# Kernel tuning notes

Hardware: AMD Instinct MI355X
Metric: run time of the kernel (lower is better)

Reference implementation:

```python
import jax, jax.numpy as jnp
import numpy as np

BN_EPS = 1e-5
L2_EPS = 1e-12


def _gconv(x, adj, W, b):
    # x: [B, N, F_in], adj: [N, N] (densified sparse), W: [F_in, F_out]
    y = jnp.einsum('rc,bcf->brf', adj, x)          # sparse aggregation (spmm)
    y = jnp.einsum('brf,fo->bro', y, W) + b        # dense transform + bias
    n = jnp.sqrt(jnp.sum(y * y, axis=2, keepdims=True))
    return y / jnp.maximum(n, L2_EPS)              # F.normalize(p=2, dim=2)


def _bn3(x):
    # BatchNorm1d over channel dim=1 (roinum), batch stats, affine = identity
    m = jnp.mean(x, axis=(0, 2), keepdims=True)
    v = jnp.var(x, axis=(0, 2), keepdims=True)
    return (x - m) / jnp.sqrt(v + BN_EPS)


def _bn2(x):
    m = jnp.mean(x, axis=0, keepdims=True)
    v = jnp.var(x, axis=0, keepdims=True)
    return (x - m) / jnp.sqrt(v + BN_EPS)


def setup_inputs() -> dict:
    key = jax.random.key(0)
    ks = jax.random.split(key, 20)
    B, N, F_in, H, E, L = 256, 400, 400, 64, 64, 2
    NNZ = 16000
    pred_in = H * 2 + E  # hidden*(num_layers-1) + embedding = 192
    nhid = H

    def xavier(k, fi, fo):
        s = np.sqrt(6.0 / (fi + fo))
        return jax.random.uniform(k, (fi, fo), jnp.float32, -s, s)

    return {
        'x': jax.random.normal(ks[0], (B, N, F_in), jnp.float32),
        'adj_rows': jax.random.randint(ks[1], (NNZ,), 0, N, jnp.int32),
        'adj_cols': jax.random.randint(ks[2], (NNZ,), 0, N, jnp.int32),
        'adj_vals': jax.random.uniform(ks[3], (NNZ,), jnp.float32),
        'W1': xavier(ks[4], F_in, H), 'b1': jnp.zeros((H,), jnp.float32),
        'W2': xavier(ks[5], H, H),    'b2': jnp.zeros((H,), jnp.float32),
        'W3': xavier(ks[6], H, E),    'b3': jnp.zeros((E,), jnp.float32),
        'fc1_W': xavier(ks[7], pred_in, nhid), 'fc1_b': jnp.zeros((nhid,), jnp.float32),
        'fc2_W': xavier(ks[8], nhid, nhid),    'fc2_b': jnp.zeros((nhid,), jnp.float32),
        'fc3_W': xavier(ks[9], nhid, L),       'fc3_b': jnp.zeros((L,), jnp.float32),
    }


def reference(x, adj_rows, adj_cols, adj_vals,
              W1, b1, W2, b2, W3, b3,
              fc1_W, fc1_b, fc2_W, fc2_b, fc3_W, fc3_b):
    N = x.shape[1]
    adj = jnp.zeros((N, N), x.dtype).at[adj_rows, adj_cols].add(adj_vals)

    x1 = _bn3(jax.nn.relu(_gconv(x, adj, W1, b1)))
    out1 = jnp.max(x1, axis=1)                     # [B, H]
    x2 = _bn3(jax.nn.relu(_gconv(x1, adj, W2, b2)))
    out2 = jnp.max(x2, axis=1)                     # [B, H]
    x3 = _gconv(x2, adj, W3, b3)                   # [B, N, E]
    out3 = jnp.max(x3, axis=1)                     # [B, E]

    h = jnp.concatenate([out1, out2, out3], axis=1)  # [B, 2H+E]
    h = _bn2(jax.nn.relu(h @ fc1_W + fc1_b))
    h = _bn2(jax.nn.relu(h @ fc2_W + fc2_b))
    ypred = h @ fc3_W + fc3_b
    return ypred, x3
```

## Files before the change

### kernel.cpp

```cpp
#include <hip/hip_runtime.h>
#include <hip/hip_bf16.h>
#include <math.h>

#define Bb   256
#define Nn   400
#define FIN  400
#define Hh   64
#define NNZ  16000
#define Mrows (Bb*Nn)
#define KP   416
#define UTP  416
#define BH_COUNT 16384.0f

typedef unsigned int  u32x2 __attribute__((ext_vector_type(2)));
typedef unsigned int  u32x4 __attribute__((ext_vector_type(4)));
typedef __bf16        bf16x8 __attribute__((ext_vector_type(8)));
typedef float         f32x4 __attribute__((ext_vector_type(4)));

__device__ __forceinline__ unsigned int f2bf(float x) {
    unsigned int u = __builtin_bit_cast(unsigned int, x);
    return (u + 0x7FFFu + ((u >> 16) & 1u)) >> 16;
}
__device__ __forceinline__ float bf2f(unsigned int h) {
    unsigned int u = h << 16;
    return __builtin_bit_cast(float, u);
}

__global__ void initk(float* __restrict__ Adf, float* __restrict__ stats,
                      unsigned short* __restrict__ Ut) {
    int t = blockIdx.x * blockDim.x + threadIdx.x;
    if (t < Nn * KP) Adf[t] = 0.f;
    if (t < 1600) stats[t] = 0.f;
    if (t < Bb * Hh * 16) {
        int bh = t >> 4, k = Nn + (t & 15);
        Ut[(size_t)bh * UTP + k] = 0;
    }
}

__global__ void scatAk(const int* __restrict__ rows, const int* __restrict__ cols,
                       const float* __restrict__ vals, float* __restrict__ Adf) {
    int i = blockIdx.x * blockDim.x + threadIdx.x;
    if (i < NNZ) atomicAdd(&Adf[rows[i] * KP + cols[i]], vals[i]);
}

__global__ void cvtAk(const float* __restrict__ Adf, unsigned short* __restrict__ Adbf) {
    int i = blockIdx.x * blockDim.x + threadIdx.x;
    if (i < Nn * KP) Adbf[i] = (unsigned short)f2bf(Adf[i]);
}

__global__ __launch_bounds__(256) void wprep(
        const float* __restrict__ W1, const float* __restrict__ W2,
        const float* __restrict__ W3,
        unsigned short* __restrict__ T1h, unsigned short* __restrict__ T1l,
        unsigned short* __restrict__ T2h, unsigned short* __restrict__ T2l,
        unsigned short* __restrict__ T3h, unsigned short* __restrict__ T3l) {
    const int w = blockIdx.x >> 6;
    const int c = blockIdx.x & 63;
    const float* W = (w == 0) ? W1 : (w == 1) ? W2 : W3;
    const int KT   = (w == 0) ? FIN : Hh;
    const int KPAD = (w == 0) ? 416 : 64;
    unsigned short* Th = (w == 0) ? T1h : (w == 1) ? T2h : T3h;
    unsigned short* Tl = (w == 0) ? T1l : (w == 1) ? T2l : T3l;

    for (int k = threadIdx.x; k < KPAD; k += 256) {
        float v = (k < KT) ? W[k * 64 + c] : 0.f;
        unsigned int hb = f2bf(v);
        Th[c * KPAD + k] = (unsigned short)hb;
        Tl[c * KPAD + k] = (unsigned short)f2bf(v - bf2f(hb));
    }
}

__global__ __launch_bounds__(256) void xg400(
        const float* __restrict__ A,
        const unsigned short* __restrict__ Wth,
        const unsigned short* __restrict__ Wtl,
        unsigned short* __restrict__ Ut) {
    const int tid  = threadIdx.x;
    const int wv   = tid >> 6;
    const int lane = tid & 63;
    const int cl   = lane & 15;
    const int g    = lane >> 4;
    const int m0   = blockIdx.x * 128;
    const int rowA = m0 + wv * 32 + cl;
    const int rowB = rowA + 16;

    f32x4 acc[2][4];
#pragma unroll
    for (int t2 = 0; t2 < 2; ++t2)
#pragma unroll
        for (int n = 0; n < 4; ++n) acc[t2][n] = f32x4{0.f, 0.f, 0.f, 0.f};

    auto loadA = [&](int s, float4& l0, float4& h0, float4& l1, float4& h1) {
        int kk = s * 32 + g * 8;
        int kc = kk > 392 ? 392 : kk;
        const float* p = &A[(size_t)rowA * FIN + kc];
        l0 = *reinterpret_cast<const float4*>(p);
        h0 = *reinterpret_cast<const float4*>(p + 4);
        const float* q = &A[(size_t)rowB * FIN + kc];
        l1 = *reinterpret_cast<const float4*>(q);
        h1 = *reinterpret_cast<const float4*>(q + 4);
    };
    auto loadW = [&](int s, u32x4* dst) {
        int kk = s * 32 + g * 8;
#pragma unroll
        for (int n = 0; n < 4; ++n) {
            dst[n]     = *reinterpret_cast<const u32x4*>(&Wth[(size_t)(n * 16 + cl) * 416 + kk]);
            dst[4 + n] = *reinterpret_cast<const u32x4*>(&Wtl[(size_t)(n * 16 + cl) * 416 + kk]);
        }
    };
    auto split = [&](const float4& lo, const float4& hi, bf16x8& ah, bf16x8& al) {
        float v0 = lo.x, v1 = lo.y, v2 = lo.z, v3 = lo.w;
        float v4 = hi.x, v5 = hi.y, v6 = hi.z, v7 = hi.w;
        unsigned h0, h1;
        u32x4 hw, lw;
        h0 = f2bf(v0); h1 = f2bf(v1);
        hw[0] = h0 | (h1 << 16);
        lw[0] = f2bf(v0 - bf2f(h0)) | (f2bf(v1 - bf2f(h1)) << 16);
        h0 = f2bf(v2); h1 = f2bf(v3);
        hw[1] = h0 | (h1 << 16);
        lw[1] = f2bf(v2 - bf2f(h0)) | (f2bf(v3 - bf2f(h1)) << 16);
        h0 = f2bf(v4); h1 = f2bf(v5);
        hw[2] = h0 | (h1 << 16);
        lw[2] = f2bf(v4 - bf2f(h0)) | (f2bf(v5 - bf2f(h1)) << 16);
        h0 = f2bf(v6); h1 = f2bf(v7);
        hw[3] = h0 | (h1 << 16);
        lw[3] = f2bf(v6 - bf2f(h0)) | (f2bf(v7 - bf2f(h1)) << 16);
        ah = __builtin_bit_cast(bf16x8, hw);
        al = __builtin_bit_cast(bf16x8, lw);
    };

    float4 cAl0, cAh0, cAl1, cAh1, nAl0, nAh0, nAl1, nAh1;
    u32x4  cW[8], nW[8];
    loadA(0, cAl0, cAh0, cAl1, cAh1);
    loadW(0, cW);

    for (int s = 0; s < 13; ++s) {
        if (s < 12) {
            loadA(s + 1, nAl0, nAh0, nAl1, nAh1);
            loadW(s + 1, nW);
        }
        bf16x8 ah0, al0, ah1, al1;
        split(cAl0, cAh0, ah0, al0);
        split(cAl1, cAh1, ah1, al1);
#pragma unroll
        for (int n = 0; n < 4; ++n) {
            bf16x8 bh = __builtin_bit_cast(bf16x8, cW[n]);
            bf16x8 bl = __builtin_bit_cast(bf16x8, cW[4 + n]);
            acc[0][n] = __builtin_amdgcn_mfma_f32_16x16x32_bf16(ah0, bh, acc[0][n], 0, 0, 0);
            acc[0][n] = __builtin_amdgcn_mfma_f32_16x16x32_bf16(ah0, bl, acc[0][n], 0, 0, 0);
            acc[0][n] = __builtin_amdgcn_mfma_f32_16x16x32_bf16(al0, bh, acc[0][n], 0, 0, 0);
            acc[1][n] = __builtin_amdgcn_mfma_f32_16x16x32_bf16(ah1, bh, acc[1][n], 0, 0, 0);
            acc[1][n] = __builtin_amdgcn_mfma_f32_16x16x32_bf16(ah1, bl, acc[1][n], 0, 0, 0);
            acc[1][n] = __builtin_amdgcn_mfma_f32_16x16x32_bf16(al1, bh, acc[1][n], 0, 0, 0);
        }
        if (s < 12) {
            cAl0 = nAl0; cAh0 = nAh0; cAl1 = nAl1; cAh1 = nAh1;
#pragma unroll
            for (int j = 0; j < 8; ++j) cW[j] = nW[j];
        }
    }

#pragma unroll
    for (int t2 = 0; t2 < 2; ++t2) {
        const int row0  = m0 + wv * 32 + t2 * 16 + g * 4;
        const int b     = row0 / Nn;
        const int node0 = row0 - b * Nn;
#pragma unroll
        for (int n = 0; n < 4; ++n) {
            const int col = n * 16 + cl;
            u32x2 pk;
            pk[0] = f2bf(acc[t2][n][0]) | (f2bf(acc[t2][n][1]) << 16);
            pk[1] = f2bf(acc[t2][n][2]) | (f2bf(acc[t2][n][3]) << 16);
            *reinterpret_cast<u32x2*>(&Ut[((size_t)b * 64 + col) * UTP + node0]) = pk;
        }
    }
}

__global__ __launch_bounds__(512) void xgb(
        const float* __restrict__ Z,
        const unsigned short* __restrict__ Wth,
        const unsigned short* __restrict__ Wtl,
        const float* __restrict__ mean, const float* __restrict__ inv,
        unsigned short* __restrict__ Ut,
        float* __restrict__ outmax) {
    __shared__ float smax[8][64];
    const int b    = blockIdx.x;
    const int tid  = threadIdx.x;
    const int wv   = tid >> 6;
    const int lane = tid & 63;
    const int cl   = lane & 15;
    const int g    = lane >> 4;

    float vmax[16];
#pragma unroll
    for (int j = 0; j < 16; ++j) vmax[j] = -3.4e38f;

    for (int i = 0; i < 4; ++i) {
        const int t = wv + 8 * i;
        if (t < 25) {
            const int node = t * 16 + cl;
            const float mm = mean[node], iv = inv[node];

            float za[16];
#pragma unroll
            for (int s = 0; s < 2; ++s) {
                const float* p = &Z[((size_t)b * Nn + node) * 64 + s * 32 + g * 8];
                float4 lo = *reinterpret_cast<const float4*>(p);
                float4 hi = *reinterpret_cast<const float4*>(p + 4);
                za[s * 8 + 0] = (lo.x - mm) * iv;
                za[s * 8 + 1] = (lo.y - mm) * iv;
                za[s * 8 + 2] = (lo.z - mm) * iv;
                za[s * 8 + 3] = (lo.w - mm) * iv;
                za[s * 8 + 4] = (hi.x - mm) * iv;
                za[s * 8 + 5] = (hi.y - mm) * iv;
                za[s * 8 + 6] = (hi.z - mm) * iv;
                za[s * 8 + 7] = (hi.w - mm) * iv;
            }
#pragma unroll
            for (int j = 0; j < 16; ++j) vmax[j] = fmaxf(vmax[j], za[j]);

            f32x4 acc[4];
#pragma unroll
            for (int n = 0; n < 4; ++n) acc[n] = f32x4{0.f, 0.f, 0.f, 0.f};

#pragma unroll
            for (int s = 0; s < 2; ++s) {
                u32x4 hw, lw;
#pragma unroll
                for (int j = 0; j < 4; ++j) {
                    unsigned h0 = f2bf(za[s * 8 + 2 * j]);
                    unsigned h1 = f2bf(za[s * 8 + 2 * j + 1]);
                    hw[j] = h0 | (h1 << 16);
                    lw[j] = f2bf(za[s * 8 + 2 * j] - bf2f(h0)) |
                            (f2bf(za[s * 8 + 2 * j + 1] - bf2f(h1)) << 16);
                }
                bf16x8 ah = __builtin_bit_cast(bf16x8, hw);
                bf16x8 al = __builtin_bit_cast(bf16x8, lw);
                const int kk = s * 32 + g * 8;
#pragma unroll
                for (int n = 0; n < 4; ++n) {
                    u32x4 bhw = *reinterpret_cast<const u32x4*>(&Wth[(size_t)(n * 16 + cl) * 64 + kk]);
                    u32x4 blw = *reinterpret_cast<const u32x4*>(&Wtl[(size_t)(n * 16 + cl) * 64 + kk]);
                    bf16x8 bh = __builtin_bit_cast(bf16x8, bhw);
                    bf16x8 bl = __builtin_bit_cast(bf16x8, blw);
                    acc[n] = __builtin_amdgcn_mfma_f32_16x16x32_bf16(ah, bh, acc[n], 0, 0, 0);
                    acc[n] = __builtin_amdgcn_mfma_f32_16x16x32_bf16(ah, bl, acc[n], 0, 0, 0);
                    acc[n] = __builtin_amdgcn_mfma_f32_16x16x32_bf16(al, bh, acc[n], 0, 0, 0);
                }
            }

            const int node0 = t * 16 + g * 4;
#pragma unroll
            for (int n = 0; n < 4; ++n) {
                const int col = n * 16 + cl;
                u32x2 pk;
                pk[0] = f2bf(acc[n][0]) | (f2bf(acc[n][1]) << 16);
                pk[1] = f2bf(acc[n][2]) | (f2bf(acc[n][3]) << 16);
                *reinterpret_cast<u32x2*>(&Ut[((size_t)b * 64 + col) * UTP + node0]) = pk;
            }
        }
    }

#pragma unroll
    for (int m = 1; m < 16; m <<= 1)
#pragma unroll
        for (int j = 0; j < 16; ++j)
            vmax[j] = fmaxf(vmax[j], __shfl_xor(vmax[j], m));
    if (cl == 0) {
#pragma unroll
        for (int j = 0; j < 16; ++j) {
            const int h = 32 * (j >> 3) + g * 8 + (j & 7);
            smax[wv][h] = vmax[j];
        }
    }
    __syncthreads();
    if (tid < 64) {
        float m = smax[0][tid];
#pragma unroll
        for (int w = 1; w < 8; ++w) m = fmaxf(m, smax[w][tid]);
        outmax[b * 64 + tid] = m;
    }
}

template <bool STATS>
__global__ __launch_bounds__(256) void aggmm(
        const unsigned short* __restrict__ Ad,
        const unsigned short* __restrict__ Ut,
        const float* __restrict__ bias,
        float* __restrict__ Zout,
        float* __restrict__ ssum, float* __restrict__ ssq,
        float* __restrict__ pmaxq) {
    const int b    = blockIdx.x >> 2;
    const int q    = blockIdx.x & 3;
    const int tid  = threadIdx.x;
    const int lane = tid & 63;
    const int wv   = tid >> 6;
    const int cl   = lane & 15;
    const int g    = lane >> 4;
    const unsigned short* __restrict__ Ub = Ut + (size_t)b * 64 * UTP;

    f32x4 acc[2][4];
#pragma unroll
    for (int i = 0; i < 2; ++i)
#pragma unroll
        for (int n = 0; n < 4; ++n) acc[i][n] = f32x4{0.f, 0.f, 0.f, 0.f};

    for (int k0 = 0; k0 < KP; k0 += 32) {
        const int kk = k0 + g * 8;
        bf16x8 bf[4];
#pragma unroll
        for (int n = 0; n < 4; ++n) {
            u32x4 w = *reinterpret_cast<const u32x4*>(&Ub[(size_t)(n * 16 + cl) * UTP + kk]);
            bf[n] = __builtin_bit_cast(bf16x8, w);
        }
#pragma unroll
        for (int i = 0; i < 2; ++i) {
            const int t = q + 4 * wv + 16 * i;
            if (t < 25) {
                const int row = t * 16 + cl;
                u32x4 ar = *reinterpret_cast<const u32x4*>(&Ad[(size_t)row * KP + kk]);
                bf16x8 af = __builtin_bit_cast(bf16x8, ar);
#pragma unroll
                for (int n = 0; n < 4; ++n)
                    acc[i][n] = __builtin_amdgcn_mfma_f32_16x16x32_bf16(
                        af, bf[n], acc[i][n], 0, 0, 0);
            }
        }
    }

    float bv[4];
#pragma unroll
    for (int n = 0; n < 4; ++n) bv[n] = bias[n * 16 + cl];

    float pmax[4];
#pragma unroll
    for (int n = 0; n < 4; ++n) pmax[n] = -3.4e38f;

#pragma unroll
    for (int i = 0; i < 2; ++i) {
        const int t = q + 4 * wv + 16 * i;
        if (t < 25) {
            float y[4][4];
#pragma unroll
            for (int n = 0; n < 4; ++n)
#pragma unroll
                for (int r = 0; r < 4; ++r) y[n][r] = acc[i][n][r] + bv[n];

            float pss[4];
#pragma unroll
            for (int r = 0; r < 4; ++r)
                pss[r] = y[0][r]*y[0][r] + y[1][r]*y[1][r] +
                         y[2][r]*y[2][r] + y[3][r]*y[3][r];
#pragma unroll
            for (int m = 1; m < 16; m <<= 1)
#pragma unroll
                for (int r = 0; r < 4; ++r) pss[r] += __shfl_xor(pss[r], m);

            float rin[4];
#pragma unroll
            for (int r = 0; r < 4; ++r)
                rin[r] = 1.f / fmaxf(sqrtf(pss[r]), 1e-12f);

#pragma unroll
            for (int n = 0; n < 4; ++n)
#pragma unroll
                for (int r = 0; r < 4; ++r) {
                    float z = y[n][r] * rin[r];
                    if (STATS) z = fmaxf(z, 0.f);
                    y[n][r] = z;
                    const int row = t * 16 + g * 4 + r;
                    Zout[((size_t)b * Nn + row) * Hh + n * 16 + cl] = z;
                    if (!STATS) pmax[n] = fmaxf(pmax[n], z);
                }

            if (STATS) {
                float s1[4], s2[4];
#pragma unroll
                for (int r = 0; r < 4; ++r) {
                    s1[r] = y[0][r] + y[1][r] + y[2][r] + y[3][r];
                    s2[r] = y[0][r]*y[0][r] + y[1][r]*y[1][r] +
                            y[2][r]*y[2][r] + y[3][r]*y[3][r];
                }
#pragma unroll
                for (int m = 1; m < 16; m <<= 1)
#pragma unroll
                    for (int r = 0; r < 4; ++r) {
                        s1[r] += __shfl_xor(s1[r], m);
                        s2[r] += __shfl_xor(s2[r], m);
                    }
                if (cl == 0) {
#pragma unroll
                    for (int r = 0; r < 4; ++r) {
                        const int row = t * 16 + g * 4 + r;
                        atomicAdd(&ssum[row], s1[r]);
                        atomicAdd(&ssq[row],  s2[r]);
                    }
                }
            }
        }
    }

    if constexpr (!STATS) {
        __shared__ float sm[4][64];
#pragma unroll
        for (int m = 16; m < 64; m <<= 1)
#pragma unroll
            for (int n = 0; n < 4; ++n)
                pmax[n] = fmaxf(pmax[n], __shfl_xor(pmax[n], m));
        if (lane < 16) {
#pragma unroll
            for (int n = 0; n < 4; ++n) sm[wv][n * 16 + cl] = pmax[n];
        }
        __syncthreads();
        if (tid < 64) {
            float m = fmaxf(fmaxf(sm[0][tid], sm[1][tid]),
                            fmaxf(sm[2][tid], sm[3][tid]));
            pmaxq[(size_t)blockIdx.x * 64 + tid] = m;
        }
    }
}

__global__ void red4max(const float* __restrict__ pmaxq, float* __restrict__ out3) {
    const int b = blockIdx.x, h = threadIdx.x;
    float m = pmaxq[(size_t)(b * 4 + 0) * 64 + h];
    m = fmaxf(m, pmaxq[(size_t)(b * 4 + 1) * 64 + h]);
    m = fmaxf(m, pmaxq[(size_t)(b * 4 + 2) * 64 + h]);
    m = fmaxf(m, pmaxq[(size_t)(b * 4 + 3) * 64 + h]);
    out3[b * 64 + h] = m;
}

__global__ void finalize_stats(const float* __restrict__ ssum,
                               const float* __restrict__ ssq,
                               float* __restrict__ mean, float* __restrict__ inv) {
    int r = threadIdx.x;
    if (r < Nn) {
        float m = ssum[r] * (1.0f / BH_COUNT);
        float v = ssq[r] * (1.0f / BH_COUNT) - m * m;
        mean[r] = m;
        inv[r]  = rsqrtf(v + 1e-5f);
    }
}

__global__ __launch_bounds__(1024) void headk(
        const float* __restrict__ out1, const float* __restrict__ out2,
        const float* __restrict__ out3,
        const float* __restrict__ W1f, const float* __restrict__ b1f,
        const float* __restrict__ W2f, const float* __restrict__ b2f,
        const float* __restrict__ W3f, const float* __restrict__ b3f,
        float* __restrict__ ypred) {
    __shared__ float gA[256][64];
    __shared__ float w1s[192 * 64];
    __shared__ float w2s[64 * 64];
    __shared__ float mS[64], iS[64];
    const int t = threadIdx.x;
    const int r = t >> 2, q = t & 3;

    for (int i = t; i < 192 * 64; i += 1024) w1s[i] = W1f[i];
    for (int i = t; i < 64 * 64; i += 1024) w2s[i] = W2f[i];
    __syncthreads();

    float acc[16];
#pragma unroll
    for (int j = 0; j < 16; ++j) acc[j] = b1f[q * 16 + j];
    for (int k = 0; k < 192; ++k) {
        float hv = (k < 64) ? out1[r * 64 + k]
                 : (k < 128) ? out2[r * 64 + (k - 64)]
                             : out3[r * 64 + (k - 128)];
#pragma unroll
        for (int j = 0; j < 16; ++j) acc[j] += hv * w1s[k * 64 + q * 16 + j];
    }
#pragma unroll
    for (int j = 0; j < 16; ++j) gA[r][q * 16 + j] = fmaxf(acc[j], 0.f);
    __syncthreads();

    if (t < 64) {
        float s = 0.f, s2 = 0.f;
        for (int rr = 0; rr < 256; ++rr) { float v = gA[rr][t]; s += v; s2 += v * v; }
        float m = s * (1.f / 256.f);
        float var = s2 * (1.f / 256.f) - m * m;
        mS[t] = m;
        iS[t] = rsqrtf(var + 1e-5f);
    }
    __syncthreads();

#pragma unroll
    for (int j = 0; j < 16; ++j) acc[j] = b2f[q * 16 + j];
#pragma unroll
    for (int k = 0; k < 64; ++k) {
        float gn = (gA[r][k] - mS[k]) * iS[k];
#pragma unroll
        for (int j = 0; j < 16; ++j) acc[j] += gn * w2s[k * 64 + q * 16 + j];
    }
    __syncthreads();
#pragma unroll
    for (int j = 0; j < 16; ++j) gA[r][q * 16 + j] = fmaxf(acc[j], 0.f);
    __syncthreads();

    if (t < 64) {
        float s = 0.f, s2 = 0.f;
        for (int rr = 0; rr < 256; ++rr) { float v = gA[rr][t]; s += v; s2 += v * v; }
        float m = s * (1.f / 256.f);
        float var = s2 * (1.f / 256.f) - m * m;
        mS[t] = m;
        iS[t] = rsqrtf(var + 1e-5f);
    }
    __syncthreads();

    if (q < 2) {
        float a = b3f[q];
#pragma unroll
        for (int k = 0; k < 64; ++k) {
            float gn = (gA[r][k] - mS[k]) * iS[k];
            a += gn * W3f[k * 2 + q];
        }
        ypred[r * 2 + q] = a;
    }
}

extern "C" void kernel_launch(void* const* d_in, const int* in_sizes, int n_in,
                              void* d_out, int out_size, void* d_ws, size_t ws_size,
                              hipStream_t stream) {
    const float* x    = (const float*)d_in[0];
    const int*   arow = (const int*)d_in[1];
    const int*   acol = (const int*)d_in[2];
    const float* aval = (const float*)d_in[3];
    const float* W1 = (const float*)d_in[4];
    const float* b1 = (const float*)d_in[5];
    const float* W2 = (const float*)d_in[6];
    const float* b2 = (const float*)d_in[7];
    const float* W3 = (const float*)d_in[8];
    const float* b3 = (const float*)d_in[9];
    const float* fc1W = (const float*)d_in[10];
    const float* fc1b = (const float*)d_in[11];
    const float* fc2W = (const float*)d_in[12];
    const float* fc2b = (const float*)d_in[13];
    const float* fc3W = (const float*)d_in[14];
    const float* fc3b = (const float*)d_in[15];

    char* w = (char*)d_ws;
    size_t off = 0;
    float* Adf = (float*)(w + off);            off += (size_t)Nn * KP * 4;
    unsigned short* Adbf = (unsigned short*)(w + off); off += (size_t)Nn * KP * 2;
    unsigned short* T1h = (unsigned short*)(w + off); off += (size_t)64 * 416 * 2;
    unsigned short* T1l = (unsigned short*)(w + off); off += (size_t)64 * 416 * 2;
    unsigned short* T2h = (unsigned short*)(w + off); off += (size_t)64 * 64 * 2;
    unsigned short* T2l = (unsigned short*)(w + off); off += (size_t)64 * 64 * 2;
    unsigned short* T3h = (unsigned short*)(w + off); off += (size_t)64 * 64 * 2;
    unsigned short* T3l = (unsigned short*)(w + off); off += (size_t)64 * 64 * 2;
    unsigned short* Ut = (unsigned short*)(w + off); off += (size_t)Bb * 64 * UTP * 2;
    float* Z = (float*)(w + off);              off += (size_t)Mrows * Hh * 4;
    float* stats = (float*)(w + off);          off += 1600 * 4;
    float* ssum1 = stats, *ssq1 = stats + 400, *ssum2 = stats + 800, *ssq2 = stats + 1200;
    float* mean1 = (float*)(w + off); off += 1600;
    float* inv1  = (float*)(w + off); off += 1600;
    float* mean2 = (float*)(w + off); off += 1600;
    float* inv2  = (float*)(w + off); off += 1600;
    float* out1  = (float*)(w + off); off += Bb * Hh * 4;
    float* out2  = (float*)(w + off); off += Bb * Hh * 4;
    float* out3  = (float*)(w + off); off += Bb * Hh * 4;
    float* pmaxq = (float*)(w + off); off += (size_t)Bb * 4 * 64 * 4;

    float* ypred = (float*)d_out;
    float* x3    = (float*)d_out + 512;

    initk<<<384, 1024, 0, stream>>>(Adf, stats, Ut);
    scatAk<<<(NNZ + 255) / 256, 256, 0, stream>>>(arow, acol, aval, Adf);
    cvtAk<<<(Nn * KP + 1023) / 1024, 1024, 0, stream>>>(Adf, Adbf);
    wprep<<<192, 256, 0, stream>>>(W1, W2, W3, T1h, T1l, T2h, T2l, T3h, T3l);

    xg400<<<Mrows / 128, 256, 0, stream>>>(x, T1h, T1l, Ut);
    aggmm<true><<<Bb * 4, 256, 0, stream>>>(Adbf, Ut, b1, Z, ssum1, ssq1, nullptr);
    finalize_stats<<<1, 512, 0, stream>>>(ssum1, ssq1, mean1, inv1);

    xgb<<<Bb, 512, 0, stream>>>(Z, T2h, T2l, mean1, inv1, Ut, out1);
    aggmm<true><<<Bb * 4, 256, 0, stream>>>(Adbf, Ut, b2, Z, ssum2, ssq2, nullptr);
    finalize_stats<<<1, 512, 0, stream>>>(ssum2, ssq2, mean2, inv2);

    xgb<<<Bb, 512, 0, stream>>>(Z, T3h, T3l, mean2, inv2, Ut, out2);
    aggmm<false><<<Bb * 4, 256, 0, stream>>>(Adbf, Ut, b3, x3, nullptr, nullptr, pmaxq);
    red4max<<<Bb, 64, 0, stream>>>(pmaxq, out3);

    headk<<<1, 1024, 0, stream>>>(out1, out2, out3, fc1W, fc1b, fc2W, fc2b,
                                  fc3W, fc3b, ypred);
}
```

Baseline: 318.4 us.

## Fuse per-batch dense transform with adjacency aggregation through shared memory

Layers 2 and 3 now run a single fused kernel per batch. It computes the BN-normalized feature transform into an LDS-resident transposed tile, then does the adjacency aggregation, L2 normalization and stats/max reduction from that tile. This removes the global round trip of the intermediate Ut buffer, two kernel launches per layer, and the separate red4max pass. The cost is a large LDS footprint (about 54KB), one block per batch (256 blocks, so less parallelism than the 1024-block aggmm), and separate Z1/Z2 buffers because the kernel reads and writes Z in the same launch.

```diff
diff --git a/kernel.cpp b/kernel.cpp
--- a/kernel.cpp
+++ b/kernel.cpp
@@ -10,6 +10,7 @@
 #define Mrows (Bb*Nn)
 #define KP   416
 #define UTP  416
+#define UPAD 420
 #define BH_COUNT 16384.0f
 
 typedef unsigned int  u32x2 __attribute__((ext_vector_type(2)));
@@ -176,14 +177,137 @@
     }
 }
 
-__global__ __launch_bounds__(512) void xgb(
-        const float* __restrict__ Z,
+__global__ __launch_bounds__(256) void aggmm(
+        const unsigned short* __restrict__ Ad,
+        const unsigned short* __restrict__ Ut,
+        const float* __restrict__ bias,
+        float* __restrict__ Zout,
+        float* __restrict__ ssum, float* __restrict__ ssq) {
+    const int b    = blockIdx.x >> 2;
+    const int q    = blockIdx.x & 3;
+    const int tid  = threadIdx.x;
+    const int lane = tid & 63;
+    const int wv   = tid >> 6;
+    const int cl   = lane & 15;
+    const int g    = lane >> 4;
+    const unsigned short* __restrict__ Ub = Ut + (size_t)b * 64 * UTP;
+
+    f32x4 acc[2][4];
+#pragma unroll
+    for (int i = 0; i < 2; ++i)
+#pragma unroll
+        for (int n = 0; n < 4; ++n) acc[i][n] = f32x4{0.f, 0.f, 0.f, 0.f};
+
+    for (int k0 = 0; k0 < KP; k0 += 32) {
+        const int kk = k0 + g * 8;
+        bf16x8 bf[4];
+#pragma unroll
+        for (int n = 0; n < 4; ++n) {
+            u32x4 w = *reinterpret_cast<const u32x4*>(&Ub[(size_t)(n * 16 + cl) * UTP + kk]);
+            bf[n] = __builtin_bit_cast(bf16x8, w);
+        }
+#pragma unroll
+        for (int i = 0; i < 2; ++i) {
+            const int t = q + 4 * wv + 16 * i;
+            if (t < 25) {
+                const int row = t * 16 + cl;
+                u32x4 ar = *reinterpret_cast<const u32x4*>(&Ad[(size_t)row * KP + kk]);
+                bf16x8 af = __builtin_bit_cast(bf16x8, ar);
+#pragma unroll
+                for (int n = 0; n < 4; ++n)
+                    acc[i][n] = __builtin_amdgcn_mfma_f32_16x16x32_bf16(
+                        af, bf[n], acc[i][n], 0, 0, 0);
+            }
+        }
+    }
+
+    float bv[4];
+#pragma unroll
+    for (int n = 0; n < 4; ++n) bv[n] = bias[n * 16 + cl];
+
+#pragma unroll
+    for (int i = 0; i < 2; ++i) {
+        const int t = q + 4 * wv + 16 * i;
+        if (t < 25) {
+            float y[4][4];
+#pragma unroll
+            for (int n = 0; n < 4; ++n)
+#pragma unroll
+                for (int r = 0; r < 4; ++r) y[n][r] = acc[i][n][r] + bv[n];
+
+            float pss[4];
+#pragma unroll
+            for (int r = 0; r < 4; ++r)
+                pss[r] = y[0][r]*y[0][r] + y[1][r]*y[1][r] +
+                         y[2][r]*y[2][r] + y[3][r]*y[3][r];
+#pragma unroll
+            for (int m = 1; m < 16; m <<= 1)
+#pragma unroll
+                for (int r = 0; r < 4; ++r) pss[r] += __shfl_xor(pss[r], m);
+
+            float rin[4];
+#pragma unroll
+            for (int r = 0; r < 4; ++r)
+                rin[r] = 1.f / fmaxf(sqrtf(pss[r]), 1e-12f);
+
+            float s1[4], s2[4];
+#pragma unroll
+            for (int r = 0; r < 4; ++r) { s1[r] = 0.f; s2[r] = 0.f; }
+#pragma unroll
+            for (int n = 0; n < 4; ++n)
+#pragma unroll
+                for (int r = 0; r < 4; ++r) {
+                    float z = fmaxf(y[n][r] * rin[r], 0.f);
+                    const int row = t * 16 + g * 4 + r;
+                    Zout[((size_t)b * Nn + row) * Hh + n * 16 + cl] = z;
+                    s1[r] += z;
+                    s2[r] += z * z;
+                }
+#pragma unroll
+            for (int m = 1; m < 16; m <<= 1)
+#pragma unroll
+                for (int r = 0; r < 4; ++r) {
+                    s1[r] += __shfl_xor(s1[r], m);
+                    s2[r] += __shfl_xor(s2[r], m);
+                }
+            if (cl == 0) {
+#pragma unroll
+                for (int r = 0; r < 4; ++r) {
+                    const int row = t * 16 + g * 4 + r;
+                    atomicAdd(&ssum[row], s1[r]);
+                    atomicAdd(&ssq[row],  s2[r]);
+                }
+            }
+        }
+    }
+}
+
+__global__ void finalize_stats(const float* __restrict__ ssum,
+                               const float* __restrict__ ssq,
+                               float* __restrict__ mean, float* __restrict__ inv) {
+    int r = threadIdx.x;
+    if (r < Nn) {
+        float m = ssum[r] * (1.0f / BH_COUNT);
+        float v = ssq[r] * (1.0f / BH_COUNT) - m * m;
+        mean[r] = m;
+        inv[r]  = rsqrtf(v + 1e-5f);
+    }
+}
+
+template <bool STATS>
+__global__ __launch_bounds__(512) void fusedl(
+        const float* __restrict__ Zin,
+        const unsigned short* __restrict__ Ad,
         const unsigned short* __restrict__ Wth,
         const unsigned short* __restrict__ Wtl,
         const float* __restrict__ mean, const float* __restrict__ inv,
-        unsigned short* __restrict__ Ut,
-        float* __restrict__ outmax) {
-    __shared__ float smax[8][64];
+        const float* __restrict__ bias,
+        float* __restrict__ Zout,
+        float* __restrict__ ssum, float* __restrict__ ssq,
+        float* __restrict__ outmax_za,
+        float* __restrict__ out3) {
+    __shared__ unsigned short Us[64 * UPAD];
+    __shared__ float sred[8][64];
     const int b    = blockIdx.x;
     const int tid  = threadIdx.x;
     const int wv   = tid >> 6;
@@ -191,6 +315,11 @@
     const int cl   = lane & 15;
     const int g    = lane >> 4;
 
+    for (int i = tid; i < 64 * (UPAD - Nn); i += 512) {
+        int c = i / (UPAD - Nn), k = Nn + i % (UPAD - Nn);
+        Us[c * UPAD + k] = 0;
+    }
+
     float vmax[16];
 #pragma unroll
     for (int j = 0; j < 16; ++j) vmax[j] = -3.4e38f;
@@ -204,7 +333,7 @@
             float za[16];
 #pragma unroll
             for (int s = 0; s < 2; ++s) {
-                const float* p = &Z[((size_t)b * Nn + node) * 64 + s * 32 + g * 8];
+                const float* p = &Zin[((size_t)b * Nn + node) * 64 + s * 32 + g * 8];
                 float4 lo = *reinterpret_cast<const float4*>(p);
                 float4 hi = *reinterpret_cast<const float4*>(p + 4);
                 za[s * 8 + 0] = (lo.x - mm) * iv;
@@ -256,7 +385,7 @@
                 u32x2 pk;
                 pk[0] = f2bf(acc[n][0]) | (f2bf(acc[n][1]) << 16);
                 pk[1] = f2bf(acc[n][2]) | (f2bf(acc[n][3]) << 16);
-                *reinterpret_cast<u32x2*>(&Ut[((size_t)b * 64 + col) * UTP + node0]) = pk;
+                *reinterpret_cast<u32x2*>(&Us[col * UPAD + node0]) = pk;
             }
         }
     }
@@ -270,130 +399,113 @@
 #pragma unroll
         for (int j = 0; j < 16; ++j) {
             const int h = 32 * (j >> 3) + g * 8 + (j & 7);
-            smax[wv][h] = vmax[j];
+            sred[wv][h] = vmax[j];
         }
     }
     __syncthreads();
     if (tid < 64) {
-        float m = smax[0][tid];
-#pragma unroll
-        for (int w = 1; w < 8; ++w) m = fmaxf(m, smax[w][tid]);
-        outmax[b * 64 + tid] = m;
-    }
-}
-
-template <bool STATS>
-__global__ __launch_bounds__(256) void aggmm(
-        const unsigned short* __restrict__ Ad,
-        const unsigned short* __restrict__ Ut,
-        const float* __restrict__ bias,
-        float* __restrict__ Zout,
-        float* __restrict__ ssum, float* __restrict__ ssq,
-        float* __restrict__ pmaxq) {
-    const int b    = blockIdx.x >> 2;
-    const int q    = blockIdx.x & 3;
-    const int tid  = threadIdx.x;
-    const int lane = tid & 63;
-    const int wv   = tid >> 6;
-    const int cl   = lane & 15;
-    const int g    = lane >> 4;
-    const unsigned short* __restrict__ Ub = Ut + (size_t)b * 64 * UTP;
-
-    f32x4 acc[2][4];
-#pragma unroll
-    for (int i = 0; i < 2; ++i)
-#pragma unroll
-        for (int n = 0; n < 4; ++n) acc[i][n] = f32x4{0.f, 0.f, 0.f, 0.f};
-
-    for (int k0 = 0; k0 < KP; k0 += 32) {
-        const int kk = k0 + g * 8;
-        bf16x8 bf[4];
-#pragma unroll
-        for (int n = 0; n < 4; ++n) {
-            u32x4 w = *reinterpret_cast<const u32x4*>(&Ub[(size_t)(n * 16 + cl) * UTP + kk]);
-            bf[n] = __builtin_bit_cast(bf16x8, w);
-        }
+        float m = sred[0][tid];
+#pragma unroll
+        for (int w = 1; w < 8; ++w) m = fmaxf(m, sred[w][tid]);
+        outmax_za[b * 64 + tid] = m;
+    }
+
+    const float bv0 = bias[cl],      bv1 = bias[16 + cl],
+                bv2 = bias[32 + cl], bv3 = bias[48 + cl];
+    float pmax[4];
+#pragma unroll
+    for (int n = 0; n < 4; ++n) pmax[n] = -3.4e38f;
+
+#pragma unroll
+    for (int s2 = 0; s2 < 2; ++s2) {
+        f32x4 acc[2][4];
+#pragma unroll
+        for (int i = 0; i < 2; ++i)
+#pragma unroll
+            for (int n = 0; n < 4; ++n) acc[i][n] = f32x4{0.f, 0.f, 0.f, 0.f};
+
+        for (int k0 = 0; k0 < KP; k0 += 32) {
+            const int kk = k0 + g * 8;
+            bf16x8 bf[4];
+#pragma unroll
+            for (int n = 0; n < 4; ++n) {
+                const unsigned short* p = &Us[(n * 16 + cl) * UPAD + kk];
+                u32x2 lo = *reinterpret_cast<const u32x2*>(p);
+                u32x2 hi = *reinterpret_cast<const u32x2*>(p + 4);
+                u32x4 w; w[0] = lo[0]; w[1] = lo[1]; w[2] = hi[0]; w[3] = hi[1];
+                bf[n] = __builtin_bit_cast(bf16x8, w);
+            }
+#pragma unroll
+            for (int i = 0; i < 2; ++i) {
+                const int t = wv + 8 * (i + 2 * s2);
+                if (t < 25) {
+                    const int row = t * 16 + cl;
+                    u32x4 ar = *reinterpret_cast<const u32x4*>(&Ad[(size_t)row * KP + kk]);
+                    bf16x8 af = __builtin_bit_cast(bf16x8, ar);
+#pragma unroll
+                    for (int n = 0; n < 4; ++n)
+                        acc[i][n] = __builtin_amdgcn_mfma_f32_16x16x32_bf16(
+                            af, bf[n], acc[i][n], 0, 0, 0);
+                }
+            }
+        }
+
 #pragma unroll
         for (int i = 0; i < 2; ++i) {
-            const int t = q + 4 * wv + 16 * i;
+            const int t = wv + 8 * (i + 2 * s2);
             if (t < 25) {
-                const int row = t * 16 + cl;
-                u32x4 ar = *reinterpret_cast<const u32x4*>(&Ad[(size_t)row * KP + kk]);
-                bf16x8 af = __builtin_bit_cast(bf16x8, ar);
+                float y[4][4];
+                const float bvs[4] = {bv0, bv1, bv2, bv3};
 #pragma unroll
                 for (int n = 0; n < 4; ++n)
-                    acc[i][n] = __builtin_amdgcn_mfma_f32_16x16x32_bf16(
-                        af, bf[n], acc[i][n], 0, 0, 0);
-            }
-        }
-    }
-
-    float bv[4];
-#pragma unroll
-    for (int n = 0; n < 4; ++n) bv[n] = bias[n * 16 + cl];
-
-    float pmax[4];
-#pragma unroll
-    for (int n = 0; n < 4; ++n) pmax[n] = -3.4e38f;
-
-#pragma unroll
-    for (int i = 0; i < 2; ++i) {
-        const int t = q + 4 * wv + 16 * i;
-        if (t < 25) {
-            float y[4][4];
-#pragma unroll
-            for (int n = 0; n < 4; ++n)
-#pragma unroll
-                for (int r = 0; r < 4; ++r) y[n][r] = acc[i][n][r] + bv[n];
-
-            float pss[4];
-#pragma unroll
-            for (int r = 0; r < 4; ++r)
-                pss[r] = y[0][r]*y[0][r] + y[1][r]*y[1][r] +
-                         y[2][r]*y[2][r] + y[3][r]*y[3][r];
-#pragma unroll
-            for (int m = 1; m < 16; m <<= 1)
-#pragma unroll
-                for (int r = 0; r < 4; ++r) pss[r] += __shfl_xor(pss[r], m);
-
-            float rin[4];
-#pragma unroll
-            for (int r = 0; r < 4; ++r)
-                rin[r] = 1.f / fmaxf(sqrtf(pss[r]), 1e-12f);
-
-#pragma unroll
-            for (int n = 0; n < 4; ++n)
-#pragma unroll
-                for (int r = 0; r < 4; ++r) {
-                    float z = y[n][r] * rin[r];
-                    if (STATS) z = fmaxf(z, 0.f);
-                    y[n][r] = z;
-                    const int row = t * 16 + g * 4 + r;
-                    Zout[((size_t)b * Nn + row) * Hh + n * 16 + cl] = z;
-                    if (!STATS) pmax[n] = fmaxf(pmax[n], z);
-                }
-
-            if (STATS) {
-                float s1[4], s2[4];
-#pragma unroll
-                for (int r = 0; r < 4; ++r) {
-                    s1[r] = y[0][r] + y[1][r] + y[2][r] + y[3][r];
-                    s2[r] = y[0][r]*y[0][r] + y[1][r]*y[1][r] +
-                            y[2][r]*y[2][r] + y[3][r]*y[3][r];
-                }
+#pragma unroll
+                    for (int r = 0; r < 4; ++r) y[n][r] = acc[i][n][r] + bvs[n];
+
+                float pss[4];
+#pragma unroll
+                for (int r = 0; r < 4; ++r)
+                    pss[r] = y[0][r]*y[0][r] + y[1][r]*y[1][r] +
+                             y[2][r]*y[2][r] + y[3][r]*y[3][r];
 #pragma unroll
                 for (int m = 1; m < 16; m <<= 1)
 #pragma unroll
+                    for (int r = 0; r < 4; ++r) pss[r] += __shfl_xor(pss[r], m);
+
+                float rin[4];
+#pragma unroll
+                for (int r = 0; r < 4; ++r)
+                    rin[r] = 1.f / fmaxf(sqrtf(pss[r]), 1e-12f);
+
+                float s1[4], s2a[4];
+#pragma unroll
+                for (int r = 0; r < 4; ++r) { s1[r] = 0.f; s2a[r] = 0.f; }
+#pragma unroll
+                for (int n = 0; n < 4; ++n)
+#pragma unroll
                     for (int r = 0; r < 4; ++r) {
-                        s1[r] += __shfl_xor(s1[r], m);
-                        s2[r] += __shfl_xor(s2[r], m);
+                        float z = y[n][r] * rin[r];
+                        if (STATS) z = fmaxf(z, 0.f);
+                        const int row = t * 16 + g * 4 + r;
+                        Zout[((size_t)b * Nn + row) * Hh + n * 16 + cl] = z;
+                        if (STATS) { s1[r] += z; s2a[r] += z * z; }
+                        else        pmax[n] = fmaxf(pmax[n], z);
                     }
-                if (cl == 0) {
-#pragma unroll
-                    for (int r = 0; r < 4; ++r) {
-                        const int row = t * 16 + g * 4 + r;
-                        atomicAdd(&ssum[row], s1[r]);
-                        atomicAdd(&ssq[row],  s2[r]);
+
+                if (STATS) {
+#pragma unroll
+                    for (int m = 1; m < 16; m <<= 1)
+#pragma unroll
+                        for (int r = 0; r < 4; ++r) {
+                            s1[r]  += __shfl_xor(s1[r], m);
+                            s2a[r] += __shfl_xor(s2a[r], m);
+                        }
+                    if (cl == 0) {
+#pragma unroll
+                        for (int r = 0; r < 4; ++r) {
+                            const int row = t * 16 + g * 4 + r;
+                            atomicAdd(&ssum[row], s1[r]);
+                            atomicAdd(&ssq[row],  s2a[r]);
+                        }
                     }
                 }
             }
@@ -401,7 +513,7 @@
     }
 
     if constexpr (!STATS) {
-        __shared__ float sm[4][64];
+        __syncthreads();
 #pragma unroll
         for (int m = 16; m < 64; m <<= 1)
 #pragma unroll
@@ -409,35 +521,15 @@
                 pmax[n] = fmaxf(pmax[n], __shfl_xor(pmax[n], m));
         if (lane < 16) {
 #pragma unroll
-            for (int n = 0; n < 4; ++n) sm[wv][n * 16 + cl] = pmax[n];
+            for (int n = 0; n < 4; ++n) sred[wv][n * 16 + cl] = pmax[n];
         }
         __syncthreads();
         if (tid < 64) {
-            float m = fmaxf(fmaxf(sm[0][tid], sm[1][tid]),
-                            fmaxf(sm[2][tid], sm[3][tid]));
-            pmaxq[(size_t)blockIdx.x * 64 + tid] = m;
-        }
-    }
-}
-
-__global__ void red4max(const float* __restrict__ pmaxq, float* __restrict__ out3) {
-    const int b = blockIdx.x, h = threadIdx.x;
-    float m = pmaxq[(size_t)(b * 4 + 0) * 64 + h];
-    m = fmaxf(m, pmaxq[(size_t)(b * 4 + 1) * 64 + h]);
-    m = fmaxf(m, pmaxq[(size_t)(b * 4 + 2) * 64 + h]);
-    m = fmaxf(m, pmaxq[(size_t)(b * 4 + 3) * 64 + h]);
-    out3[b * 64 + h] = m;
-}
-
-__global__ void finalize_stats(const float* __restrict__ ssum,
-                               const float* __restrict__ ssq,
-                               float* __restrict__ mean, float* __restrict__ inv) {
-    int r = threadIdx.x;
-    if (r < Nn) {
-        float m = ssum[r] * (1.0f / BH_COUNT);
-        float v = ssq[r] * (1.0f / BH_COUNT) - m * m;
-        mean[r] = m;
-        inv[r]  = rsqrtf(v + 1e-5f);
+            float m = sred[0][tid];
+#pragma unroll
+            for (int w = 1; w < 8; ++w) m = fmaxf(m, sred[w][tid]);
+            out3[b * 64 + tid] = m;
+        }
     }
 }
 
@@ -548,7 +640,8 @@
     unsigned short* T3h = (unsigned short*)(w + off); off += (size_t)64 * 64 * 2;
     unsigned short* T3l = (unsigned short*)(w + off); off += (size_t)64 * 64 * 2;
     unsigned short* Ut = (unsigned short*)(w + off); off += (size_t)Bb * 64 * UTP * 2;
-    float* Z = (float*)(w + off);              off += (size_t)Mrows * Hh * 4;
+    float* Z1 = (float*)(w + off);             off += (size_t)Mrows * Hh * 4;
+    float* Z2 = (float*)(w + off);             off += (size_t)Mrows * Hh * 4;
     float* stats = (float*)(w + off);          off += 1600 * 4;
     float* ssum1 = stats, *ssq1 = stats + 400, *ssum2 = stats + 800, *ssq2 = stats + 1200;
     float* mean1 = (float*)(w + off); off += 1600;
@@ -558,7 +651,6 @@
     float* out1  = (float*)(w + off); off += Bb * Hh * 4;
     float* out2  = (float*)(w + off); off += Bb * Hh * 4;
     float* out3  = (float*)(w + off); off += Bb * Hh * 4;
-    float* pmaxq = (float*)(w + off); off += (size_t)Bb * 4 * 64 * 4;
 
     float* ypred = (float*)d_out;
     float* x3    = (float*)d_out + 512;
@@ -569,16 +661,15 @@
     wprep<<<192, 256, 0, stream>>>(W1, W2, W3, T1h, T1l, T2h, T2l, T3h, T3l);
 
     xg400<<<Mrows / 128, 256, 0, stream>>>(x, T1h, T1l, Ut);
-    aggmm<true><<<Bb * 4, 256, 0, stream>>>(Adbf, Ut, b1, Z, ssum1, ssq1, nullptr);
+    aggmm<<<Bb * 4, 256, 0, stream>>>(Adbf, Ut, b1, Z1, ssum1, ssq1);
     finalize_stats<<<1, 512, 0, stream>>>(ssum1, ssq1, mean1, inv1);
 
-    xgb<<<Bb, 512, 0, stream>>>(Z, T2h, T2l, mean1, inv1, Ut, out1);
-    aggmm<true><<<Bb * 4, 256, 0, stream>>>(Adbf, Ut, b2, Z, ssum2, ssq2, nullptr);
+    fusedl<true><<<Bb, 512, 0, stream>>>(Z1, Adbf, T2h, T2l, mean1, inv1, b2,
+                                         Z2, ssum2, ssq2, out1, nullptr);
     finalize_stats<<<1, 512, 0, stream>>>(ssum2, ssq2, mean2, inv2);
 
-    xgb<<<Bb, 512, 0, stream>>>(Z, T3h, T3l, mean2, inv2, Ut, out2);
-    aggmm<false><<<Bb * 4, 256, 0, stream>>>(Adbf, Ut, b3, x3, nullptr, nullptr, pmaxq);
-    red4max<<<Bb, 64, 0, stream>>>(pmaxq, out3);
+    fusedl<false><<<Bb, 512, 0, stream>>>(Z2, Adbf, T3h, T3l, mean2, inv2, b3,
+                                          x3, nullptr, nullptr, out2, out3);
 
     headk<<<1, 1024, 0, stream>>>(out1, out2, out3, fc1W, fc1b, fc2W, fc2b,
                                   fc3W, fc3b, ypred);
```

Result: faster. 305.1 us (-4.2%).
